# Kernel optimization log

Measured on AMD Instinct MI355X. Metric: run time of the kernel, lower is better.

Reference implementation:

```python
import jax, jax.numpy as jnp
import numpy as np

TOP_K = 2
EPS = 1e-10


def setup_inputs() -> dict:
    key = jax.random.key(0)
    k1, k2, k3, k4 = jax.random.split(key, 4)
    B, S, H, E = 4, 2048, 1024, 8
    tokens = jax.random.normal(k1, (B, S, H), dtype=jnp.float32)
    router_w = jax.random.normal(k2, (E, H), dtype=jnp.float32) * (1.0 / np.sqrt(H))
    router_b = jax.random.normal(k3, (E,), dtype=jnp.float32) * 0.01
    expert_weights = jax.random.normal(k4, (E, H, H), dtype=jnp.float32) * (1.0 / np.sqrt(H))
    return {"tokens": tokens, "router_w": router_w, "router_b": router_b,
            "expert_weights": expert_weights}


def reference(tokens, router_w, router_b, expert_weights):
    B, S, H = tokens.shape
    E = expert_weights.shape[0]
    # Router (torch Linear: x @ W^T + b)
    logits = jnp.einsum('bsh,eh->bse', tokens, router_w) + router_b  # [B,S,E]
    probs = jax.nn.softmax(logits, axis=-1)
    top_p, top_i = jax.lax.top_k(probs, TOP_K)            # [B,S,K]
    w = top_p / (jnp.sum(top_p, axis=-1, keepdims=True) + EPS)  # normalized weights

    x = tokens.reshape(-1, H)                              # [N,H]
    idx = top_i.reshape(-1, TOP_K)                         # [N,K]
    wf = w.reshape(-1, TOP_K)                              # [N,K]

    # Expert GEMM: compute all experts then gather selected (dense, vectorized
    # equivalent of the sort/pad/grouped-GEMM dispatch; padded rows with
    # original_indices==-1 never contribute to the output).
    y_all = jnp.einsum('nh,ehd->ned', x, expert_weights)   # [N,E,H]
    y_k = jnp.take_along_axis(y_all, idx[:, :, None], axis=1)  # [N,K,H]

    out = jnp.einsum('nk,nkh->nh', wf, y_k)                # weighted combine
    acc = jnp.clip(jnp.sum(wf, axis=-1), EPS, None)        # weight accumulator
    out = (out / acc[:, None]).reshape(B, S, H)

    # epsilon scale tying output to normalized router probs (gradient path)
    scale = 1.0 + jnp.sum(w, axis=-1, keepdims=True) * EPS  # [B,S,1]
    return out * scale
```

## Files before the change

### kernel.cpp

```cpp
#include <hip/hip_runtime.h>
#include <stdint.h>

#define N_TOK 8192
#define H_DIM 1024
#define N_EXP 8
#define MAX_TILES 136

typedef __bf16 bf16x8 __attribute__((ext_vector_type(8)));
typedef float floatx4 __attribute__((ext_vector_type(4)));

typedef __attribute__((address_space(1))) void GV;
typedef __attribute__((address_space(3))) void LV;

static __device__ __forceinline__ unsigned short f2b(float f) {
    union { float f; unsigned int i; } v; v.f = f;
    unsigned int u = v.i;
    return (unsigned short)((u + 0x7FFFu + ((u >> 16) & 1u)) >> 16);
}

__global__ __launch_bounds__(256) void k_front(
    const float* __restrict__ tokens,
    const float* __restrict__ router_w,
    const float* __restrict__ router_b,
    const float* __restrict__ W,
    int* __restrict__ sel, float* __restrict__ w_arr,
    unsigned short* __restrict__ tokb,
    unsigned short* __restrict__ Bp)
{
    __shared__ __align__(16) unsigned short sm[8 * H_DIM];
    const int t = threadIdx.x;

    if (blockIdx.x >= 2048) {
        const int idx = blockIdx.x - 2048;
        const int kg = idx & 127;
        const int e  = idx >> 7;
        const float* src = W + ((size_t)e * H_DIM + kg * 8) * H_DIM;
#pragma unroll
        for (int i = 0; i < 8; ++i) {
            int p = (i * 256 + t) * 4;
            float4 v = *(const float4*)(src + p);
            sm[p + 0] = f2b(v.x); sm[p + 1] = f2b(v.y);
            sm[p + 2] = f2b(v.z); sm[p + 3] = f2b(v.w);
        }
        __syncthreads();
        unsigned short* dst = Bp + (size_t)(e * 128 + kg) * H_DIM * 8;
#pragma unroll
        for (int i = 0; i < 4; ++i) {
            int d = i * 256 + t;
            unsigned short v[8];
#pragma unroll
            for (int j = 0; j < 8; ++j) v[j] = sm[j * H_DIM + d];
            *(uint4*)(dst + (size_t)d * 8) = *(uint4*)v;
        }
        return;
    }

    const int wave = t >> 6;
    const int lane = t & 63;
    const int n = blockIdx.x * 4 + wave;

    const float* xp = tokens + (size_t)n * H_DIM + lane * 16;
    float x[16];
#pragma unroll
    for (int i = 0; i < 4; ++i) {
        float4 v = *(const float4*)(xp + i * 4);
        x[i * 4 + 0] = v.x; x[i * 4 + 1] = v.y; x[i * 4 + 2] = v.z; x[i * 4 + 3] = v.w;
    }

    {
        unsigned short xb[16];
#pragma unroll
        for (int j = 0; j < 16; ++j) xb[j] = f2b(x[j]);
        unsigned short* dp = tokb + (size_t)n * H_DIM + lane * 16;
        *(uint4*)(dp)     = *(uint4*)(xb);
        *(uint4*)(dp + 8) = *(uint4*)(xb + 8);
    }

    float acc[N_EXP];
#pragma unroll
    for (int e = 0; e < N_EXP; ++e) {
        const float* wp = router_w + e * H_DIM + lane * 16;
        float s = 0.f;
#pragma unroll
        for (int i = 0; i < 4; ++i) {
            float4 v = *(const float4*)(wp + i * 4);
            s += x[i * 4 + 0] * v.x + x[i * 4 + 1] * v.y
               + x[i * 4 + 2] * v.z + x[i * 4 + 3] * v.w;
        }
        acc[e] = s;
    }

#pragma unroll
    for (int e = 0; e < N_EXP; ++e) {
        float a = acc[e];
#pragma unroll
        for (int off = 32; off > 0; off >>= 1) a += __shfl_xor(a, off);
        acc[e] = a;
    }

    if (lane == 0) {
        float lg[N_EXP];
#pragma unroll
        for (int e = 0; e < N_EXP; ++e) lg[e] = acc[e] + router_b[e];
        int e0 = 0;
#pragma unroll
        for (int e = 1; e < N_EXP; ++e) if (lg[e] > lg[e0]) e0 = e;
        int e1 = -1;
#pragma unroll
        for (int e = 0; e < N_EXP; ++e) {
            if (e == e0) continue;
            if (e1 < 0 || lg[e] > lg[e1]) e1 = e;
        }
        float w0 = 1.f / (1.f + __expf(lg[e1] - lg[e0]));
        float w1 = 1.f - w0;
        sel[n] = e0 | (e1 << 4);
        w_arr[n * 2] = w0;
        w_arr[n * 2 + 1] = w1;
    }
}

__global__ __launch_bounds__(256) void k_scan(
    const int* __restrict__ sel, int* __restrict__ cnt, int* __restrict__ bucket)
{
    __shared__ int ssel[N_TOK + N_TOK / 32];
    __shared__ int sc[256];
    const int e = blockIdx.x;
    const int t = threadIdx.x;
#pragma unroll
    for (int i = 0; i < 32; ++i) {
        int n = i * 256 + t;
        ssel[n + (n >> 5)] = sel[n];
    }
    __syncthreads();
    const int base = t * 32;
    int c = 0;
#pragma unroll
    for (int i = 0; i < 32; ++i) {
        int n = base + i;
        int s = ssel[n + (n >> 5)];
        c += ((s & 15) == e) + (((s >> 4) & 15) == e);
    }
    sc[t] = c;
    __syncthreads();
    for (int off = 1; off < 256; off <<= 1) {
        int v = (t >= off) ? sc[t - off] : 0;
        __syncthreads();
        sc[t] += v;
        __syncthreads();
    }
    int pos = sc[t] - c;
    if (t == 255) cnt[e] = sc[255];
#pragma unroll
    for (int i = 0; i < 32; ++i) {
        int n = base + i;
        int s = ssel[n + (n >> 5)];
        if ((s & 15) == e)        bucket[e * N_TOK + pos++] = 2 * n;
        if (((s >> 4) & 15) == e) bucket[e * N_TOK + pos++] = 2 * n + 1;
    }
}

__global__ __launch_bounds__(256, 4) void k_gemm(
    const unsigned short* __restrict__ tokb,
    const unsigned short* __restrict__ Bp,
    const int* __restrict__ cnt, const int* __restrict__ bucket,
    const float* __restrict__ w_arr,
    float* __restrict__ out)
{
    const int nt = blockIdx.x & 7;
    const int tile = blockIdx.x >> 3;
    int base = 0, e = 0, mt = -1;
#pragma unroll
    for (int ee = 0; ee < 8; ++ee) {
        int te = (cnt[ee] + 127) >> 7;
        if (tile >= base && tile < base + te) { e = ee; mt = tile - base; }
        base += te;
    }
    if (mt < 0) return;
    const int cnt_local = cnt[e] - mt * 128;

    __shared__ __align__(16) unsigned short Asm[128 * 64];
    __shared__ __align__(16) unsigned short Bsm[8 * 128 * 8];
    __shared__ int rows[128];
    __shared__ float wrow[128];

    const int t = threadIdx.x;
    if (t < 128) {
        int rid = (t < cnt_local) ? bucket[e * N_TOK + mt * 128 + t] : -1;
        rows[t] = rid;
        wrow[t] = (rid >= 0) ? w_arr[rid] : 0.f;
    }
    __syncthreads();

    const int wv = t >> 6, lane = t & 63;
    const int d0 = nt * 128;

    const int p_sw = (lane & 7) ^ ((lane >> 3) & 7);
    const unsigned short* aptr[4];
#pragma unroll
    for (int i = 0; i < 4; ++i) {
        int r = i * 32 + wv * 8 + (lane >> 3);
        int rid = rows[r];
        int tok = (rid >= 0) ? (rid >> 1) : 0;
        aptr[i] = tokb + (size_t)tok * H_DIM + p_sw * 8;
    }
    const unsigned short* bbase = Bp
        + ((size_t)(e * 128 + (t >> 7)) * H_DIM + d0 + (t & 127)) * 8;

    const int w_row = wv >> 1, w_col = wv & 1;
    const int m_lane = lane & 15, quad = lane >> 4;
    const int r7 = m_lane & 7;

    floatx4 acc[4][4];
#pragma unroll
    for (int i = 0; i < 4; ++i)
#pragma unroll
        for (int j = 0; j < 4; ++j) acc[i][j] = (floatx4){0.f, 0.f, 0.f, 0.f};

    for (int kt = 0; kt < H_DIM / 64; ++kt) {
#pragma unroll
        for (int i = 0; i < 4; ++i) {
            __builtin_amdgcn_global_load_lds(
                (GV*)(aptr[i] + kt * 64),
                (LV*)(&Asm[i * 2048 + wv * 512]), 16, 0, 0);
            __builtin_amdgcn_global_load_lds(
                (GV*)(bbase + (size_t)i * 16384 + (size_t)kt * 65536),
                (LV*)(&Bsm[i * 2048 + wv * 512]), 16, 0, 0);
        }
        __syncthreads();

#pragma unroll
        for (int s = 0; s < 2; ++s) {
            bf16x8 a[4], b[4];
#pragma unroll
            for (int i = 0; i < 4; ++i) {
                int row = w_row * 64 + i * 16 + m_lane;
                a[i] = *(const bf16x8*)&Asm[row * 64 + ((s * 4 + quad) ^ r7) * 8];
            }
#pragma unroll
            for (int j = 0; j < 4; ++j)
                b[j] = *(const bf16x8*)&Bsm[((s * 4 + quad) * 128 + w_col * 64 + j * 16 + m_lane) * 8];
#pragma unroll
            for (int i = 0; i < 4; ++i)
#pragma unroll
                for (int j = 0; j < 4; ++j)
                    acc[i][j] = __builtin_amdgcn_mfma_f32_16x16x32_bf16(a[i], b[j], acc[i][j], 0, 0, 0);
        }
        __syncthreads();
    }

#pragma unroll
    for (int i = 0; i < 4; ++i) {
        const int lr_base = w_row * 64 + i * 16 + quad * 4;
#pragma unroll
        for (int reg = 0; reg < 4; ++reg) {
            const int lr = lr_base + reg;
            const int rid = rows[lr];
            if (rid >= 0) {
                const float wgt = wrow[lr];
                float* op = out + (size_t)(rid >> 1) * H_DIM + d0 + w_col * 64 + m_lane;
#pragma unroll
                for (int j = 0; j < 4; ++j)
                    atomicAdd(op + j * 16, wgt * acc[i][j][reg]);
            }
        }
    }
}

extern "C" void kernel_launch(void* const* d_in, const int* in_sizes, int n_in,
                              void* d_out, int out_size, void* d_ws, size_t ws_size,
                              hipStream_t stream)
{
    const float* tokens   = (const float*)d_in[0];
    const float* router_w = (const float*)d_in[1];
    const float* router_b = (const float*)d_in[2];
    const float* W        = (const float*)d_in[3];
    float* out = (float*)d_out;

    char* ws = (char*)d_ws;
    int*   cnt    = (int*)(ws);
    int*   sel    = (int*)(ws + 1024);
    float* w_arr  = (float*)(ws + 34816);
    int*   bucket = (int*)(ws + 100352);
    unsigned short* tokb = (unsigned short*)(ws + 362496);
    unsigned short* Bp   = (unsigned short*)(ws + 17139712);

    hipMemsetAsync(out, 0, (size_t)out_size * sizeof(float), stream);
    k_front<<<2048 + 1024, 256, 0, stream>>>(tokens, router_w, router_b, W,
                                             sel, w_arr, tokb, Bp);
    k_scan <<<N_EXP, 256, 0, stream>>>(sel, cnt, bucket);
    k_gemm <<<MAX_TILES * 8, 256, 0, stream>>>(tokb, Bp, cnt, bucket, w_arr, out);
}
```

Measured before the change: 221.5 us.

## Replace atomic combine with bf16 expert output buffer and separate combine kernel

The GEMM epilogue now writes each (token, slot) result as bf16 into a per-slot buffer Y, using packed 8-byte stores. It no longer does fp32 atomicAdds into a zeroed output. A new combine kernel reads both slots per token, applies the router weights and writes the output in fp32, undoing the permuted column layout. This removes the output memset and the atomic traffic, at the cost of an extra kernel launch, an extra round trip through Y, and bf16 rounding of the expert outputs. Separately, the weight-conversion blocks in k_front now transpose in registers instead of staging through shared memory.

```diff
diff --git a/kernel.cpp b/kernel.cpp
--- a/kernel.cpp
+++ b/kernel.cpp
@@ -16,6 +16,9 @@
     union { float f; unsigned int i; } v; v.f = f;
     unsigned int u = v.i;
     return (unsigned short)((u + 0x7FFFu + ((u >> 16) & 1u)) >> 16);
+}
+static __device__ __forceinline__ float b2f(unsigned short u) {
+    union { unsigned int i; float f; } v; v.i = ((unsigned int)u) << 16; return v.f;
 }
 
 __global__ __launch_bounds__(256) void k_front(
@@ -27,30 +30,27 @@
     unsigned short* __restrict__ tokb,
     unsigned short* __restrict__ Bp)
 {
-    __shared__ __align__(16) unsigned short sm[8 * H_DIM];
     const int t = threadIdx.x;
 
     if (blockIdx.x >= 2048) {
         const int idx = blockIdx.x - 2048;
         const int kg = idx & 127;
         const int e  = idx >> 7;
-        const float* src = W + ((size_t)e * H_DIM + kg * 8) * H_DIM;
-#pragma unroll
-        for (int i = 0; i < 8; ++i) {
-            int p = (i * 256 + t) * 4;
-            float4 v = *(const float4*)(src + p);
-            sm[p + 0] = f2b(v.x); sm[p + 1] = f2b(v.y);
-            sm[p + 2] = f2b(v.z); sm[p + 3] = f2b(v.w);
-        }
-        __syncthreads();
-        unsigned short* dst = Bp + (size_t)(e * 128 + kg) * H_DIM * 8;
-#pragma unroll
-        for (int i = 0; i < 4; ++i) {
-            int d = i * 256 + t;
+        const int d  = t * 4;
+        const float* src = W + ((size_t)e * H_DIM + kg * 8) * H_DIM + d;
+        float col[8][4];
+#pragma unroll
+        for (int j = 0; j < 8; ++j) {
+            float4 v = *(const float4*)(src + (size_t)j * H_DIM);
+            col[j][0] = v.x; col[j][1] = v.y; col[j][2] = v.z; col[j][3] = v.w;
+        }
+        unsigned short* dst = Bp + ((size_t)(e * 128 + kg) * H_DIM + d) * 8;
+#pragma unroll
+        for (int k = 0; k < 4; ++k) {
             unsigned short v[8];
 #pragma unroll
-            for (int j = 0; j < 8; ++j) v[j] = sm[j * H_DIM + d];
-            *(uint4*)(dst + (size_t)d * 8) = *(uint4*)v;
+            for (int j = 0; j < 8; ++j) v[j] = f2b(col[j][k]);
+            *(uint4*)(dst + (size_t)k * 8) = *(uint4*)v;
         }
         return;
     }
@@ -163,8 +163,7 @@
     const unsigned short* __restrict__ tokb,
     const unsigned short* __restrict__ Bp,
     const int* __restrict__ cnt, const int* __restrict__ bucket,
-    const float* __restrict__ w_arr,
-    float* __restrict__ out)
+    unsigned short* __restrict__ Y)
 {
     const int nt = blockIdx.x & 7;
     const int tile = blockIdx.x >> 3;
@@ -181,14 +180,10 @@
     __shared__ __align__(16) unsigned short Asm[128 * 64];
     __shared__ __align__(16) unsigned short Bsm[8 * 128 * 8];
     __shared__ int rows[128];
-    __shared__ float wrow[128];
 
     const int t = threadIdx.x;
-    if (t < 128) {
-        int rid = (t < cnt_local) ? bucket[e * N_TOK + mt * 128 + t] : -1;
-        rows[t] = rid;
-        wrow[t] = (rid >= 0) ? w_arr[rid] : 0.f;
-    }
+    if (t < 128)
+        rows[t] = (t < cnt_local) ? bucket[e * N_TOK + mt * 128 + t] : -1;
     __syncthreads();
 
     const int wv = t >> 6, lane = t & 63;
@@ -256,13 +251,38 @@
             const int lr = lr_base + reg;
             const int rid = rows[lr];
             if (rid >= 0) {
-                const float wgt = wrow[lr];
-                float* op = out + (size_t)(rid >> 1) * H_DIM + d0 + w_col * 64 + m_lane;
-#pragma unroll
-                for (int j = 0; j < 4; ++j)
-                    atomicAdd(op + j * 16, wgt * acc[i][j][reg]);
+                unsigned short v[4];
+#pragma unroll
+                for (int j = 0; j < 4; ++j) v[j] = f2b(acc[i][j][reg]);
+                *(uint2*)(Y + (size_t)rid * H_DIM + d0 + w_col * 64 + m_lane * 4) = *(uint2*)v;
             }
         }
+    }
+}
+
+__global__ __launch_bounds__(256) void k_combine(
+    const unsigned short* __restrict__ Y, const float* __restrict__ w_arr,
+    float* __restrict__ out)
+{
+    const int g = blockIdx.x * 256 + threadIdx.x;
+    const int n = g >> 7;
+    const int c = (g & 127) * 8;
+    const unsigned short* y0 = Y + (size_t)(2 * n) * H_DIM + c;
+    const unsigned short* y1 = y0 + H_DIM;
+    uint4 a = *(const uint4*)y0;
+    uint4 b = *(const uint4*)y1;
+    const unsigned short* pa = (const unsigned short*)&a;
+    const unsigned short* pb = (const unsigned short*)&b;
+    const float w0 = w_arr[2 * n], w1 = w_arr[2 * n + 1];
+    const int seg = c >> 7;
+    const int sl0 = c & 127;
+    float* op = out + (size_t)n * H_DIM + seg * 128;
+#pragma unroll
+    for (int k = 0; k < 8; ++k) {
+        int sl = sl0 + k;
+        int wc = sl >> 6, m = (sl >> 2) & 15, j = sl & 3;
+        int d = wc * 64 + j * 16 + m;
+        op[d] = w0 * b2f(pa[k]) + w1 * b2f(pb[k]);
     }
 }
 
@@ -283,10 +303,11 @@
     int*   bucket = (int*)(ws + 100352);
     unsigned short* tokb = (unsigned short*)(ws + 362496);
     unsigned short* Bp   = (unsigned short*)(ws + 17139712);
-
-    hipMemsetAsync(out, 0, (size_t)out_size * sizeof(float), stream);
-    k_front<<<2048 + 1024, 256, 0, stream>>>(tokens, router_w, router_b, W,
-                                             sel, w_arr, tokb, Bp);
-    k_scan <<<N_EXP, 256, 0, stream>>>(sel, cnt, bucket);
-    k_gemm <<<MAX_TILES * 8, 256, 0, stream>>>(tokb, Bp, cnt, bucket, w_arr, out);
-}
+    unsigned short* Y    = (unsigned short*)(ws + 33916928);
+
+    k_front  <<<2048 + 1024, 256, 0, stream>>>(tokens, router_w, router_b, W,
+                                               sel, w_arr, tokb, Bp);
+    k_scan   <<<N_EXP, 256, 0, stream>>>(sel, cnt, bucket);
+    k_gemm   <<<MAX_TILES * 8, 256, 0, stream>>>(tokb, Bp, cnt, bucket, Y);
+    k_combine<<<N_TOK * (H_DIM / 8) / 256, 256, 0, stream>>>(Y, w_arr, out);
+}
```

After: 194.8 us. -12.1%, faster.
